# Optimization experiments

Hardware: AMD Instinct MI355X
Metric: run time of the kernel (lower is better)

Reference implementation:

```python
import jax, jax.numpy as jnp
import numpy as np

NUM_FREQS = 12  # fourfeat_config
EMB_DIM = 3 + 6 * NUM_FREQS  # identity + sin/cos per freq per dim = 75


def fourier_ipe(x, cov, decay):
    # x: [N,3], cov: [N,3,3], decay: scalar (coarse-to-fine window cutoff)
    N = x.shape[0]
    freqs = 2.0 ** jnp.arange(NUM_FREQS, dtype=jnp.float32)            # [F]
    xb = x[:, None, :] * freqs[:, None]                                # [N,F,3]
    var = jnp.diagonal(cov, axis1=-2, axis2=-1)[:, None, :] * (freqs ** 2)[:, None]  # [N,F,3]
    # nerfies-style cosine easing window per frequency band
    window = 0.5 * (1.0 - jnp.cos(jnp.pi * jnp.clip(decay - jnp.arange(NUM_FREQS, dtype=jnp.float32), 0.0, 1.0)))  # [F]
    atten = jnp.exp(-0.5 * var) * window[:, None]                      # [N,F,3]
    four = jnp.concatenate([jnp.sin(xb), jnp.cos(xb)], axis=-1) * jnp.concatenate([atten, atten], axis=-1)  # [N,F,6]
    return jnp.concatenate([x, four.reshape(N, 6 * NUM_FREQS)], axis=-1)  # [N,75]


def mlp(h, W_in, b_in, W_hid, b_hid, W_out, b_out):
    h = jax.nn.relu(h @ W_in + b_in)
    for i in range(W_hid.shape[0]):  # fixed small layer count
        h = jax.nn.relu(h @ W_hid[i] + b_hid[i])
    return h @ W_out + b_out  # output_activation = None


def setup_inputs() -> dict:
    key = jax.random.key(0)
    ks = jax.random.split(key, 16)
    bshape = (2, 16384, 8)
    mean = jax.random.normal(ks[0], (*bshape, 3), jnp.float32)
    cov = jax.random.uniform(ks[1], (*bshape, 3, 3), jnp.float32) * 1e-4  # small positive diag

    def w(k, shp):
        return jax.random.normal(k, shp, jnp.float32) / np.sqrt(shp[-2]).astype(np.float32)

    FD, FC = 256, 128  # features_density, features_color
    HD, HC = 8 - 2, 4 - 2  # n_hidden_layers = layers - 2
    return {
        'mean': mean, 'cov': cov,
        'Wd_in': w(ks[2], (EMB_DIM, FD)), 'bd_in': jnp.zeros((FD,), jnp.float32),
        'Wd_hid': w(ks[3], (HD, FD, FD)), 'bd_hid': jnp.zeros((HD, FD), jnp.float32),
        'Wd_out': w(ks[4], (FD, FD + 1)), 'bd_out': jnp.zeros((FD + 1,), jnp.float32),
        'Wc_in': w(ks[5], (FD, FC)), 'bc_in': jnp.zeros((FC,), jnp.float32),
        'Wc_hid': w(ks[6], (HC, FC, FC)), 'bc_hid': jnp.zeros((HC, FC), jnp.float32),
        'Wc_out': w(ks[7], (FC, 3)), 'bc_out': jnp.zeros((3,), jnp.float32),
        'decayscale': 12,
    }


def reference(mean, cov, Wd_in, bd_in, Wd_hid, bd_hid, Wd_out, bd_out,
              Wc_in, bc_in, Wc_hid, bc_hid, Wc_out, bc_out, decayscale):
    batch_shape = mean.shape[:-1]
    N = int(np.prod(batch_shape))
    x = mean.reshape(N, 3)
    c = cov.reshape(N, 3, 3)
    emb = fourier_ipe(x, c, jnp.float32(decayscale))                    # [N,75]
    feat = mlp(emb, Wd_in, bd_in, Wd_hid, bd_hid, Wd_out, bd_out)       # [N,257]
    d, features = feat[:, :1], feat[:, 1:]
    # parameterization == 'VolSDF' (capitalized) -> no SDF radius offset branch
    raw_rgb = mlp(features, Wc_in, bc_in, Wc_hid, bc_hid, Wc_out, bc_out)  # [N,3]
    raw = jnp.concatenate([raw_rgb, d], axis=-1)                        # [N,4]
    return raw.reshape(*batch_shape, 4)
```

## Files before the change

kernel.cpp:

```cpp
#include <hip/hip_runtime.h>
#include <hip/hip_bf16.h>

#define PI_F 3.14159265358979323846f
#define KPAD 260

typedef _Float16 h8 __attribute__((ext_vector_type(8)));
typedef _Float16 h4 __attribute__((ext_vector_type(4)));
typedef _Float16 h2 __attribute__((ext_vector_type(2)));
typedef __fp16 fp16x2 __attribute__((ext_vector_type(2)));
typedef float f32x16 __attribute__((ext_vector_type(16)));

__device__ __forceinline__ h2 cvt_pk_h2(float a, float b)
{
    fp16x2 r = __builtin_amdgcn_cvt_pkrtz(a, b);
    return __builtin_bit_cast(h2, r);
}

#define OFF_DIN   0
#define OFF_DHID  24576
#define OFF_FEAT  417792
#define OFF_CIN   483328
#define OFF_CHID  516096
#define OFF_COUT  548864
#define W_TOTAL   552960
#define FB_DIN  0
#define FB_DHID 256
#define FB_FEAT 1792
#define FB_CIN  2048
#define FB_CHID 2176
#define FB_WD0  2432
#define FB_BD0  2688
#define B_TOTAL 2689
#define PREP_TOTAL (W_TOTAL + B_TOTAL)

__global__ void prep_kernel(const float* __restrict__ Wd_in,  const float* __restrict__ Wd_hid,
                            const float* __restrict__ Wd_out, const float* __restrict__ Wc_in,
                            const float* __restrict__ Wc_hid, const float* __restrict__ Wc_out,
                            const float* __restrict__ bd_in,  const float* __restrict__ bd_hid,
                            const float* __restrict__ bd_out, const float* __restrict__ bc_in,
                            const float* __restrict__ bc_hid,
                            _Float16* __restrict__ wdst, float* __restrict__ bdst)
{
    int i = blockIdx.x * 256 + threadIdx.x;
    if (i >= PREP_TOTAL) return;
    if (i < W_TOTAL) {
        float v = 0.f;
        int j, n, k;
        #define DECODE(jj, KTv)  do { int frag = (jj) >> 3; int e = (jj) & 7;          \
                                      int lane = frag & 63; int tk = frag >> 6;         \
                                      int ntl = tk / (KTv); int kt = tk % (KTv);        \
                                      n = ntl * 32 + (lane & 31);                       \
                                      k = kt * 16 + (lane >> 5) * 8 + e; } while (0)
        if (i < OFF_DHID) {
            j = i; DECODE(j, 6);
            if (k < 75) v = Wd_in[k * 256 + n];
        } else if (i < OFF_FEAT) {
            j = i - OFF_DHID; int l = j >> 16; j &= 65535; DECODE(j, 16);
            v = Wd_hid[(l * 256 + k) * 256 + n];
        } else if (i < OFF_CIN) {
            j = i - OFF_FEAT; DECODE(j, 16);
            v = Wd_out[k * 257 + n + 1];
        } else if (i < OFF_CHID) {
            j = i - OFF_CIN; DECODE(j, 16);
            v = Wc_in[k * 128 + n];
        } else if (i < OFF_COUT) {
            j = i - OFF_CHID; int l = j >> 14; j &= 16383; DECODE(j, 8);
            v = Wc_hid[(l * 128 + k) * 128 + n];
        } else {
            j = i - OFF_COUT; DECODE(j, 8);
            if (n < 3) v = Wc_out[k * 3 + n];
        }
        #undef DECODE
        wdst[i] = (_Float16)v;
    } else {
        int b = i - W_TOTAL;
        float v = 0.f;
        #define BDECODE(bb) int ntl = (bb) >> 5; int r5 = (bb) & 31;                   \
                            int lq = r5 >> 4, jj = r5 & 15;                            \
                            int n = ntl * 32 + (jj & 3) + 8 * (jj >> 2) + 4 * lq
        if (b < FB_DHID)      { BDECODE(b); v = bd_in[n]; }
        else if (b < FB_FEAT) { int b2 = b - FB_DHID; int l = b2 >> 8; int bb = b2 & 255;
                                BDECODE(bb); v = bd_hid[l * 256 + n]; }
        else if (b < FB_CIN)  { int bb = b - FB_FEAT; BDECODE(bb); v = bd_out[n + 1]; }
        else if (b < FB_CHID) { int bb = b - FB_CIN; BDECODE(bb); v = bc_in[n]; }
        else if (b < FB_WD0)  { int b2 = b - FB_CHID; int l = b2 >> 7; int bb = b2 & 127;
                                BDECODE(bb); v = bc_hid[l * 128 + n]; }
        else if (b < FB_BD0)  { int k = b - FB_WD0; v = Wd_out[k * 257]; }
        else                  { v = bd_out[0]; }
        #undef BDECODE
        bdst[b] = v;
    }
}

__device__ __forceinline__ h8 lds_read_h8(const _Float16* p)
{
    h4 lo = *(const h4*)(p);
    h4 hi = *(const h4*)(p + 4);
    return __builtin_shufflevector(lo, hi, 0, 1, 2, 3, 4, 5, 6, 7);
}

template<int KT, int NT, bool RELU, bool DDOT>
__device__ __forceinline__ void dense(_Float16 (*At)[KPAD],
                                      const _Float16* __restrict__ WP,
                                      const float* __restrict__ bfrag,
                                      const float* __restrict__ wd0,
                                      float (*dpart)[64],
                                      int c, int lrow, int lq, int lane)
{
    const int ntile0 = c * NT;
    f32x16 acc[2][NT];
#pragma unroll
    for (int nt = 0; nt < NT; ++nt) {
        f32x16 b = *(const f32x16*)(bfrag + (ntile0 + nt) * 32 + lq * 16);
        acc[0][nt] = b;
        acc[1][nt] = b;
    }

    const _Float16* wbase = WP + ((size_t)ntile0 * KT) * 512 + (size_t)lane * 8;

#pragma unroll 2
    for (int kt = 0; kt < KT; ++kt) {
        const int koff = kt * 16 + lq * 8;
        h8 wf[NT];
#pragma unroll
        for (int nt = 0; nt < NT; ++nt)
            wf[nt] = *(const h8*)(wbase + (size_t)(nt * KT + kt) * 512);
        h8 af[2];
#pragma unroll
        for (int mt = 0; mt < 2; ++mt)
            af[mt] = lds_read_h8(&At[mt * 32 + lrow][koff]);
        __builtin_amdgcn_s_setprio(1);
#pragma unroll
        for (int mt = 0; mt < 2; ++mt)
#pragma unroll
            for (int nt = 0; nt < NT; ++nt)
                acc[mt][nt] = __builtin_amdgcn_mfma_f32_32x32x16_f16(wf[nt], af[mt], acc[mt][nt], 0, 0, 0);
        __builtin_amdgcn_s_setprio(0);
    }

    if (DDOT) {
        float s = 0.f;
        const float* w0 = wd0 + c * 64;
#pragma unroll
        for (int kk = 0; kk < 64; kk += 8) {
            h8 hv = lds_read_h8(&At[lane][c * 64 + kk]);
#pragma unroll
            for (int e = 0; e < 8; ++e)
                s = fmaf((float)hv[e], w0[kk + e], s);
        }
        dpart[c][lane] = s;
    }

    __syncthreads();

#pragma unroll
    for (int mt = 0; mt < 2; ++mt) {
        const int m = mt * 32 + lrow;
#pragma unroll
        for (int nt = 0; nt < NT; ++nt) {
#pragma unroll
            for (int p = 0; p < 4; ++p) {
                const int n0 = (ntile0 + nt) * 32 + p * 8 + lq * 4;
                h2 lo = cvt_pk_h2(acc[mt][nt][4 * p + 0], acc[mt][nt][4 * p + 1]);
                h2 hi = cvt_pk_h2(acc[mt][nt][4 * p + 2], acc[mt][nt][4 * p + 3]);
                h4 hv = __builtin_shufflevector(lo, hi, 0, 1, 2, 3);
                if (RELU) {
                    const h4 zero = {(_Float16)0, (_Float16)0, (_Float16)0, (_Float16)0};
                    hv = __builtin_elementwise_max(hv, zero);
                }
                *(h4*)(&At[m][n0]) = hv;
            }
        }
    }
    __syncthreads();
}

__global__ __launch_bounds__(256, 4)
void ffmlp_kernel(const float* __restrict__ mean, const float* __restrict__ cov,
                  const int* __restrict__ decayscale,
                  const _Float16* __restrict__ wws, const float* __restrict__ bws,
                  const float* __restrict__ bc_out,
                  float* __restrict__ out, int N)
{
    __shared__ __align__(16) _Float16 At[64][KPAD];
    __shared__ float dpart[4][64];

    const int t = threadIdx.x;
    const int c = t >> 6, lane = t & 63;
    const int lrow = lane & 31, lq = lane >> 5;
    const int p0 = blockIdx.x * 64;

    {
        const int m = t >> 2, q = t & 3;
        const long pt = (long)p0 + m;
        float x0 = 0.f, x1 = 0.f, x2 = 0.f, v0 = 0.f, v1 = 0.f, v2 = 0.f;
        if (pt < N) {
            x0 = mean[pt * 3 + 0]; x1 = mean[pt * 3 + 1]; x2 = mean[pt * 3 + 2];
            v0 = cov[pt * 9 + 0];  v1 = cov[pt * 9 + 4];  v2 = cov[pt * 9 + 8];
        }
        const float dec = (float)(*decayscale);
        if (q == 0) {
            At[m][0] = (_Float16)x0; At[m][1] = (_Float16)x1; At[m][2] = (_Float16)x2;
            for (int k = 75; k < 80; ++k) At[m][k] = (_Float16)0.f;
        } else {
            for (int k = 75 + 5 * q; k < (q == 3 ? 96 : 80 + 5 * q); ++k) At[m][k] = (_Float16)0.f;
        }
        const float xs[3] = {x0, x1, x2}, vs[3] = {v0, v1, v2};
#pragma unroll
        for (int fi = 0; fi < 3; ++fi) {
            const int f = q * 3 + fi;
            const float fs = (float)(1 << f);
            const float wcl = fminf(fmaxf(dec - (float)f, 0.f), 1.f);
            const float win = 0.5f * (1.f - cosf(wcl * PI_F));
#pragma unroll
            for (int d = 0; d < 3; ++d) {
                const float xb = xs[d] * fs;
                const float att = expf(-0.5f * vs[d] * fs * fs) * win;
                float s, co;
                sincosf(xb, &s, &co);
                At[m][3 + 6 * f + d] = (_Float16)(s * att);
                At[m][6 + 6 * f + d] = (_Float16)(co * att);
            }
        }
    }
    __syncthreads();

    dense<6, 2, true, false>(At, wws + OFF_DIN, bws + FB_DIN, bws, dpart, c, lrow, lq, lane);
#pragma unroll 1
    for (int i = 0; i < 6; ++i)
        dense<16, 2, true, false>(At, wws + OFF_DHID + i * 65536, bws + FB_DHID + i * 256,
                                  bws, dpart, c, lrow, lq, lane);
    dense<16, 2, false, true>(At, wws + OFF_FEAT, bws + FB_FEAT, bws + FB_WD0, dpart, c, lrow, lq, lane);

    dense<16, 1, true, false>(At, wws + OFF_CIN, bws + FB_CIN, bws, dpart, c, lrow, lq, lane);
#pragma unroll 1
    for (int i = 0; i < 2; ++i)
        dense<8, 1, true, false>(At, wws + OFF_CHID + i * 16384, bws + FB_CHID + i * 128,
                                 bws, dpart, c, lrow, lq, lane);

    if (c == 0) {
        f32x16 acc[2];
#pragma unroll
        for (int mt = 0; mt < 2; ++mt)
#pragma unroll
            for (int j = 0; j < 16; ++j) acc[mt][j] = 0.f;
        const _Float16* wco = wws + OFF_COUT + (size_t)lane * 8;
#pragma unroll
        for (int kt = 0; kt < 8; ++kt) {
            const int koff = kt * 16 + lq * 8;
            h8 wf = *(const h8*)(wco + (size_t)kt * 512);
#pragma unroll
            for (int mt = 0; mt < 2; ++mt) {
                h8 af = lds_read_h8(&At[mt * 32 + lrow][koff]);
                acc[mt] = __builtin_amdgcn_mfma_f32_32x32x16_f16(wf, af, acc[mt], 0, 0, 0);
            }
        }
        const float bc0 = bc_out[0], bc1 = bc_out[1], bc2 = bc_out[2];
        const float bd0 = bws[FB_BD0];
        if (lq == 0) {
#pragma unroll
            for (int mt = 0; mt < 2; ++mt) {
                const int m = mt * 32 + lrow;
                const long pt = (long)p0 + m;
                if (pt < N) {
                    float4 o;
                    o.x = acc[mt][0] + bc0;
                    o.y = acc[mt][1] + bc1;
                    o.z = acc[mt][2] + bc2;
                    o.w = dpart[0][m] + dpart[1][m] + dpart[2][m] + dpart[3][m] + bd0;
                    *(float4*)(out + pt * 4) = o;
                }
            }
        }
    }
}

extern "C" void kernel_launch(void* const* d_in, const int* in_sizes, int n_in,
                              void* d_out, int out_size, void* d_ws, size_t ws_size,
                              hipStream_t stream)
{
    const float* mean   = (const float*)d_in[0];
    const float* cov    = (const float*)d_in[1];
    const float* Wd_in  = (const float*)d_in[2];
    const float* bd_in  = (const float*)d_in[3];
    const float* Wd_hid = (const float*)d_in[4];
    const float* bd_hid = (const float*)d_in[5];
    const float* Wd_out = (const float*)d_in[6];
    const float* bd_out = (const float*)d_in[7];
    const float* Wc_in  = (const float*)d_in[8];
    const float* bc_in  = (const float*)d_in[9];
    const float* Wc_hid = (const float*)d_in[10];
    const float* bc_hid = (const float*)d_in[11];
    const float* Wc_out = (const float*)d_in[12];
    const float* bc_out = (const float*)d_in[13];
    const int*   decay  = (const int*)d_in[14];

    _Float16* wws = (_Float16*)d_ws;
    float*    bws = (float*)((char*)d_ws + (size_t)W_TOTAL * 2);

    const int N = in_sizes[0] / 3;

    const int prep_blocks = (PREP_TOTAL + 255) / 256;
    prep_kernel<<<prep_blocks, 256, 0, stream>>>(Wd_in, Wd_hid, Wd_out, Wc_in, Wc_hid, Wc_out,
                                                 bd_in, bd_hid, bd_out, bc_in, bc_hid, wws, bws);

    const int blocks = (N + 63) / 64;
    ffmlp_kernel<<<blocks, 256, 0, stream>>>(mean, cov, decay, wws, bws, bc_out, (float*)d_out, N);
}
```

Measured before the change: 315.1 us.

## Enlarge block tile to 128 rows with 2x2 wave grid for weight reuse

Each block now processes 128 points instead of 64. The four waves are arranged as two row groups by two column groups, so each wave computes 64 rows by a wider N slice (NT doubled). This halves the global weight fetches per point and increases MFMA work per weight load. In exchange it doubles LDS and accumulator registers, lowers the occupancy hint from 4 to 2 blocks per CU, and halves the block count. The DDOT and final-layer paths are reindexed to match.

```diff
diff --git a/kernel.cpp b/kernel.cpp
--- a/kernel.cpp
+++ b/kernel.cpp
@@ -104,10 +104,10 @@
                                       const _Float16* __restrict__ WP,
                                       const float* __restrict__ bfrag,
                                       const float* __restrict__ wd0,
-                                      float (*dpart)[64],
-                                      int c, int lrow, int lq, int lane)
-{
-    const int ntile0 = c * NT;
+                                      float (*dpart)[128],
+                                      int rbase, int ntile0, int wid,
+                                      int lrow, int lq, int lane)
+{
     f32x16 acc[2][NT];
 #pragma unroll
     for (int nt = 0; nt < NT; ++nt) {
@@ -128,7 +128,7 @@
         h8 af[2];
 #pragma unroll
         for (int mt = 0; mt < 2; ++mt)
-            af[mt] = lds_read_h8(&At[mt * 32 + lrow][koff]);
+            af[mt] = lds_read_h8(&At[rbase + mt * 32 + lrow][koff]);
         __builtin_amdgcn_s_setprio(1);
 #pragma unroll
         for (int mt = 0; mt < 2; ++mt)
@@ -139,23 +139,27 @@
     }
 
     if (DDOT) {
-        float s = 0.f;
-        const float* w0 = wd0 + c * 64;
-#pragma unroll
-        for (int kk = 0; kk < 64; kk += 8) {
-            h8 hv = lds_read_h8(&At[lane][c * 64 + kk]);
-#pragma unroll
-            for (int e = 0; e < 8; ++e)
-                s = fmaf((float)hv[e], w0[kk + e], s);
-        }
-        dpart[c][lane] = s;
+        const float* w0 = wd0 + wid * 64;
+#pragma unroll
+        for (int m2 = 0; m2 < 2; ++m2) {
+            const int m = lane + m2 * 64;
+            float s = 0.f;
+#pragma unroll
+            for (int kk = 0; kk < 64; kk += 8) {
+                h8 hv = lds_read_h8(&At[m][wid * 64 + kk]);
+#pragma unroll
+                for (int e = 0; e < 8; ++e)
+                    s = fmaf((float)hv[e], w0[kk + e], s);
+            }
+            dpart[wid][m] = s;
+        }
     }
 
     __syncthreads();
 
 #pragma unroll
     for (int mt = 0; mt < 2; ++mt) {
-        const int m = mt * 32 + lrow;
+        const int m = rbase + mt * 32 + lrow;
 #pragma unroll
         for (int nt = 0; nt < NT; ++nt) {
 #pragma unroll
@@ -175,23 +179,25 @@
     __syncthreads();
 }
 
-__global__ __launch_bounds__(256, 4)
+__global__ __launch_bounds__(256, 2)
 void ffmlp_kernel(const float* __restrict__ mean, const float* __restrict__ cov,
                   const int* __restrict__ decayscale,
                   const _Float16* __restrict__ wws, const float* __restrict__ bws,
                   const float* __restrict__ bc_out,
                   float* __restrict__ out, int N)
 {
-    __shared__ __align__(16) _Float16 At[64][KPAD];
-    __shared__ float dpart[4][64];
+    __shared__ __align__(16) _Float16 At[128][KPAD];
+    __shared__ float dpart[4][128];
 
     const int t = threadIdx.x;
-    const int c = t >> 6, lane = t & 63;
+    const int wid = t >> 6, lane = t & 63;
+    const int r = wid >> 1, c = wid & 1;
     const int lrow = lane & 31, lq = lane >> 5;
-    const int p0 = blockIdx.x * 64;
+    const int rbase = r * 64;
+    const int p0 = blockIdx.x * 128;
 
     {
-        const int m = t >> 2, q = t & 3;
+        const int m = t >> 1, hf = t & 1;
         const long pt = (long)p0 + m;
         float x0 = 0.f, x1 = 0.f, x2 = 0.f, v0 = 0.f, v1 = 0.f, v2 = 0.f;
         if (pt < N) {
@@ -199,16 +205,16 @@
             v0 = cov[pt * 9 + 0];  v1 = cov[pt * 9 + 4];  v2 = cov[pt * 9 + 8];
         }
         const float dec = (float)(*decayscale);
-        if (q == 0) {
+        if (hf == 0) {
             At[m][0] = (_Float16)x0; At[m][1] = (_Float16)x1; At[m][2] = (_Float16)x2;
-            for (int k = 75; k < 80; ++k) At[m][k] = (_Float16)0.f;
+            for (int k = 75; k < 86; ++k) At[m][k] = (_Float16)0.f;
         } else {
-            for (int k = 75 + 5 * q; k < (q == 3 ? 96 : 80 + 5 * q); ++k) At[m][k] = (_Float16)0.f;
+            for (int k = 86; k < 96; ++k) At[m][k] = (_Float16)0.f;
         }
         const float xs[3] = {x0, x1, x2}, vs[3] = {v0, v1, v2};
 #pragma unroll
-        for (int fi = 0; fi < 3; ++fi) {
-            const int f = q * 3 + fi;
+        for (int fi = 0; fi < 6; ++fi) {
+            const int f = hf * 6 + fi;
             const float fs = (float)(1 << f);
             const float wcl = fminf(fmaxf(dec - (float)f, 0.f), 1.f);
             const float win = 0.5f * (1.f - cosf(wcl * PI_F));
@@ -225,18 +231,21 @@
     }
     __syncthreads();
 
-    dense<6, 2, true, false>(At, wws + OFF_DIN, bws + FB_DIN, bws, dpart, c, lrow, lq, lane);
+    dense<6, 4, true, false>(At, wws + OFF_DIN, bws + FB_DIN, bws, dpart,
+                             rbase, c * 4, wid, lrow, lq, lane);
 #pragma unroll 1
     for (int i = 0; i < 6; ++i)
-        dense<16, 2, true, false>(At, wws + OFF_DHID + i * 65536, bws + FB_DHID + i * 256,
-                                  bws, dpart, c, lrow, lq, lane);
-    dense<16, 2, false, true>(At, wws + OFF_FEAT, bws + FB_FEAT, bws + FB_WD0, dpart, c, lrow, lq, lane);
-
-    dense<16, 1, true, false>(At, wws + OFF_CIN, bws + FB_CIN, bws, dpart, c, lrow, lq, lane);
+        dense<16, 4, true, false>(At, wws + OFF_DHID + i * 65536, bws + FB_DHID + i * 256,
+                                  bws, dpart, rbase, c * 4, wid, lrow, lq, lane);
+    dense<16, 4, false, true>(At, wws + OFF_FEAT, bws + FB_FEAT, bws + FB_WD0, dpart,
+                              rbase, c * 4, wid, lrow, lq, lane);
+
+    dense<16, 2, true, false>(At, wws + OFF_CIN, bws + FB_CIN, bws, dpart,
+                              rbase, c * 2, wid, lrow, lq, lane);
 #pragma unroll 1
     for (int i = 0; i < 2; ++i)
-        dense<8, 1, true, false>(At, wws + OFF_CHID + i * 16384, bws + FB_CHID + i * 128,
-                                 bws, dpart, c, lrow, lq, lane);
+        dense<8, 2, true, false>(At, wws + OFF_CHID + i * 16384, bws + FB_CHID + i * 128,
+                                 bws, dpart, rbase, c * 2, wid, lrow, lq, lane);
 
     if (c == 0) {
         f32x16 acc[2];
@@ -251,7 +260,7 @@
             h8 wf = *(const h8*)(wco + (size_t)kt * 512);
 #pragma unroll
             for (int mt = 0; mt < 2; ++mt) {
-                h8 af = lds_read_h8(&At[mt * 32 + lrow][koff]);
+                h8 af = lds_read_h8(&At[rbase + mt * 32 + lrow][koff]);
                 acc[mt] = __builtin_amdgcn_mfma_f32_32x32x16_f16(wf, af, acc[mt], 0, 0, 0);
             }
         }
@@ -260,7 +269,7 @@
         if (lq == 0) {
 #pragma unroll
             for (int mt = 0; mt < 2; ++mt) {
-                const int m = mt * 32 + lrow;
+                const int m = rbase + mt * 32 + lrow;
                 const long pt = (long)p0 + m;
                 if (pt < N) {
                     float4 o;
@@ -304,6 +313,6 @@
     prep_kernel<<<prep_blocks, 256, 0, stream>>>(Wd_in, Wd_hid, Wd_out, Wc_in, Wc_hid, Wc_out,
                                                  bd_in, bd_hid, bd_out, bc_in, bc_hid, wws, bws);
 
-    const int blocks = (N + 63) / 64;
+    const int blocks = (N + 127) / 128;
     ffmlp_kernel<<<blocks, 256, 0, stream>>>(mean, cov, decay, wws, bws, bc_out, (float*)d_out, N);
 }
```

Result: faster. 307.1 us (-2.6%).

## Double-buffer weight fragments into LDS via async global_load_lds prefetch

Applied to the files above, without the earlier changes.

Weight fragments are no longer loaded straight from global memory into registers. Each wave now uses asynchronous global-to-LDS loads into a private double buffer, prefetching the next k-tile while MFMAs run on the current one, with explicit vmcnt waits. The intent is to hide global or L2 weight-load latency behind the MFMA work. It costs 16 KB of extra LDS per block and lowers the launch-bounds occupancy hint from 4 to 3. It also depends on correct LDS ordering without a barrier, which holds only because each wave has its own buffer.

```diff
diff --git a/kernel.cpp b/kernel.cpp
--- a/kernel.cpp
+++ b/kernel.cpp
@@ -14,6 +14,13 @@
 {
     fp16x2 r = __builtin_amdgcn_cvt_pkrtz(a, b);
     return __builtin_bit_cast(h2, r);
+}
+
+__device__ __forceinline__ void stage16(const _Float16* g, _Float16* l)
+{
+    __builtin_amdgcn_global_load_lds(
+        (const __attribute__((address_space(1))) unsigned int*)g,
+        (__attribute__((address_space(3))) unsigned int*)l, 16, 0, 0);
 }
 
 #define OFF_DIN   0
@@ -101,6 +108,7 @@
 
 template<int KT, int NT, bool RELU, bool DDOT>
 __device__ __forceinline__ void dense(_Float16 (*At)[KPAD],
+                                      _Float16* __restrict__ wb,
                                       const _Float16* __restrict__ WP,
                                       const float* __restrict__ bfrag,
                                       const float* __restrict__ wd0,
@@ -116,15 +124,28 @@
         acc[1][nt] = b;
     }
 
-    const _Float16* wbase = WP + ((size_t)ntile0 * KT) * 512 + (size_t)lane * 8;
+#pragma unroll
+    for (int nt = 0; nt < NT; ++nt)
+        stage16(WP + ((size_t)((ntile0 + nt) * KT)) * 512 + lane * 8, wb + nt * 512);
 
 #pragma unroll 2
     for (int kt = 0; kt < KT; ++kt) {
+        if (kt + 1 < KT) {
+#pragma unroll
+            for (int nt = 0; nt < NT; ++nt)
+                stage16(WP + ((size_t)((ntile0 + nt) * KT + kt + 1)) * 512 + lane * 8,
+                        wb + ((kt + 1) & 1) * 1024 + nt * 512);
+            if constexpr (NT == 2) asm volatile("s_waitcnt vmcnt(2)" ::: "memory");
+            else                   asm volatile("s_waitcnt vmcnt(1)" ::: "memory");
+        } else {
+            asm volatile("s_waitcnt vmcnt(0)" ::: "memory");
+        }
+
         const int koff = kt * 16 + lq * 8;
         h8 wf[NT];
 #pragma unroll
         for (int nt = 0; nt < NT; ++nt)
-            wf[nt] = *(const h8*)(wbase + (size_t)(nt * KT + kt) * 512);
+            wf[nt] = *(const h8*)(wb + (kt & 1) * 1024 + nt * 512 + lane * 8);
         h8 af[2];
 #pragma unroll
         for (int mt = 0; mt < 2; ++mt)
@@ -175,7 +196,7 @@
     __syncthreads();
 }
 
-__global__ __launch_bounds__(256, 4)
+__global__ __launch_bounds__(256, 3)
 void ffmlp_kernel(const float* __restrict__ mean, const float* __restrict__ cov,
                   const int* __restrict__ decayscale,
                   const _Float16* __restrict__ wws, const float* __restrict__ bws,
@@ -183,12 +204,14 @@
                   float* __restrict__ out, int N)
 {
     __shared__ __align__(16) _Float16 At[64][KPAD];
+    __shared__ __align__(16) _Float16 wbuf[4][2][1024];
     __shared__ float dpart[4][64];
 
     const int t = threadIdx.x;
     const int c = t >> 6, lane = t & 63;
     const int lrow = lane & 31, lq = lane >> 5;
     const int p0 = blockIdx.x * 64;
+    _Float16* wb = &wbuf[c][0][0];
 
     {
         const int m = t >> 2, q = t & 3;
@@ -225,17 +248,18 @@
     }
     __syncthreads();
 
-    dense<6, 2, true, false>(At, wws + OFF_DIN, bws + FB_DIN, bws, dpart, c, lrow, lq, lane);
+    dense<6, 2, true, false>(At, wb, wws + OFF_DIN, bws + FB_DIN, bws, dpart, c, lrow, lq, lane);
 #pragma unroll 1
     for (int i = 0; i < 6; ++i)
-        dense<16, 2, true, false>(At, wws + OFF_DHID + i * 65536, bws + FB_DHID + i * 256,
+        dense<16, 2, true, false>(At, wb, wws + OFF_DHID + i * 65536, bws + FB_DHID + i * 256,
                                   bws, dpart, c, lrow, lq, lane);
-    dense<16, 2, false, true>(At, wws + OFF_FEAT, bws + FB_FEAT, bws + FB_WD0, dpart, c, lrow, lq, lane);
-
-    dense<16, 1, true, false>(At, wws + OFF_CIN, bws + FB_CIN, bws, dpart, c, lrow, lq, lane);
+    dense<16, 2, false, true>(At, wb, wws + OFF_FEAT, bws + FB_FEAT, bws + FB_WD0, dpart,
+                              c, lrow, lq, lane);
+
+    dense<16, 1, true, false>(At, wb, wws + OFF_CIN, bws + FB_CIN, bws, dpart, c, lrow, lq, lane);
 #pragma unroll 1
     for (int i = 0; i < 2; ++i)
-        dense<8, 1, true, false>(At, wws + OFF_CHID + i * 16384, bws + FB_CHID + i * 128,
+        dense<8, 1, true, false>(At, wb, wws + OFF_CHID + i * 16384, bws + FB_CHID + i * 128,
                                  bws, dpart, c, lrow, lq, lane);
 
     if (c == 0) {
```

New measurement: 355.7 us. 12.9% more time.

## Double-buffer weight and activation fragments across k-phases in dense layers

Applied to the files above, without the earlier changes.

Restructures the dense-layer k-loop into phases of several k-tiles with a two-slot register buffer. The global weight loads and LDS activation reads for the next phase are issued before the MFMAs of the current phase, so memory latency can overlap with matrix math. Launch bounds are relaxed from 4 to 2 blocks per SM to leave room for the larger register footprint. This trades occupancy for per-wave latency hiding.

```diff
diff --git a/kernel.cpp b/kernel.cpp
--- a/kernel.cpp
+++ b/kernel.cpp
@@ -99,7 +99,7 @@
     return __builtin_shufflevector(lo, hi, 0, 1, 2, 3, 4, 5, 6, 7);
 }
 
-template<int KT, int NT, bool RELU, bool DDOT>
+template<int KT, int PH, int NT, bool RELU, bool DDOT>
 __device__ __forceinline__ void dense(_Float16 (*At)[KPAD],
                                       const _Float16* __restrict__ WP,
                                       const float* __restrict__ bfrag,
@@ -107,7 +107,10 @@
                                       float (*dpart)[64],
                                       int c, int lrow, int lq, int lane)
 {
+    constexpr int NPH = KT / PH;
+    static_assert(NPH * PH == KT, "PH must divide KT");
     const int ntile0 = c * NT;
+
     f32x16 acc[2][NT];
 #pragma unroll
     for (int nt = 0; nt < NT; ++nt) {
@@ -116,25 +119,45 @@
         acc[1][nt] = b;
     }
 
-    const _Float16* wbase = WP + ((size_t)ntile0 * KT) * 512 + (size_t)lane * 8;
-
-#pragma unroll 2
-    for (int kt = 0; kt < KT; ++kt) {
-        const int koff = kt * 16 + lq * 8;
-        h8 wf[NT];
+    const _Float16* wbase  = WP + ((size_t)ntile0 * KT) * 512 + (size_t)lane * 8;
+    const _Float16* abase0 = &At[lrow][lq * 8];
+    const _Float16* abase1 = &At[32 + lrow][lq * 8];
+
+    h8 wfb[2][NT * PH];
+    h8 afb[2][2 * PH];
+
+#pragma unroll
+    for (int kk = 0; kk < PH; ++kk) {
 #pragma unroll
         for (int nt = 0; nt < NT; ++nt)
-            wf[nt] = *(const h8*)(wbase + (size_t)(nt * KT + kt) * 512);
-        h8 af[2];
-#pragma unroll
-        for (int mt = 0; mt < 2; ++mt)
-            af[mt] = lds_read_h8(&At[mt * 32 + lrow][koff]);
+            wfb[0][nt * PH + kk] = *(const h8*)(wbase + (size_t)(nt * KT + kk) * 512);
+        afb[0][kk]      = lds_read_h8(abase0 + kk * 16);
+        afb[0][PH + kk] = lds_read_h8(abase1 + kk * 16);
+    }
+
+#pragma unroll
+    for (int ph = 0; ph < NPH; ++ph) {
+        const int cur = ph & 1, nxt = cur ^ 1;
+        if (ph + 1 < NPH) {
+#pragma unroll
+            for (int kk = 0; kk < PH; ++kk) {
+                const int kt = (ph + 1) * PH + kk;
+#pragma unroll
+                for (int nt = 0; nt < NT; ++nt)
+                    wfb[nxt][nt * PH + kk] = *(const h8*)(wbase + (size_t)(nt * KT + kt) * 512);
+                afb[nxt][kk]      = lds_read_h8(abase0 + kt * 16);
+                afb[nxt][PH + kk] = lds_read_h8(abase1 + kt * 16);
+            }
+        }
         __builtin_amdgcn_s_setprio(1);
 #pragma unroll
-        for (int mt = 0; mt < 2; ++mt)
-#pragma unroll
-            for (int nt = 0; nt < NT; ++nt)
-                acc[mt][nt] = __builtin_amdgcn_mfma_f32_32x32x16_f16(wf[nt], af[mt], acc[mt][nt], 0, 0, 0);
+        for (int kk = 0; kk < PH; ++kk)
+#pragma unroll
+            for (int mt = 0; mt < 2; ++mt)
+#pragma unroll
+                for (int nt = 0; nt < NT; ++nt)
+                    acc[mt][nt] = __builtin_amdgcn_mfma_f32_32x32x16_f16(
+                        wfb[cur][nt * PH + kk], afb[cur][mt * PH + kk], acc[mt][nt], 0, 0, 0);
         __builtin_amdgcn_s_setprio(0);
     }
 
@@ -175,7 +198,7 @@
     __syncthreads();
 }
 
-__global__ __launch_bounds__(256, 4)
+__global__ __launch_bounds__(256, 2)
 void ffmlp_kernel(const float* __restrict__ mean, const float* __restrict__ cov,
                   const int* __restrict__ decayscale,
                   const _Float16* __restrict__ wws, const float* __restrict__ bws,
@@ -225,18 +248,19 @@
     }
     __syncthreads();
 
-    dense<6, 2, true, false>(At, wws + OFF_DIN, bws + FB_DIN, bws, dpart, c, lrow, lq, lane);
+    dense<6, 3, 2, true, false>(At, wws + OFF_DIN, bws + FB_DIN, bws, dpart, c, lrow, lq, lane);
 #pragma unroll 1
     for (int i = 0; i < 6; ++i)
-        dense<16, 2, true, false>(At, wws + OFF_DHID + i * 65536, bws + FB_DHID + i * 256,
-                                  bws, dpart, c, lrow, lq, lane);
-    dense<16, 2, false, true>(At, wws + OFF_FEAT, bws + FB_FEAT, bws + FB_WD0, dpart, c, lrow, lq, lane);
-
-    dense<16, 1, true, false>(At, wws + OFF_CIN, bws + FB_CIN, bws, dpart, c, lrow, lq, lane);
+        dense<16, 4, 2, true, false>(At, wws + OFF_DHID + i * 65536, bws + FB_DHID + i * 256,
+                                     bws, dpart, c, lrow, lq, lane);
+    dense<16, 4, 2, false, true>(At, wws + OFF_FEAT, bws + FB_FEAT, bws + FB_WD0, dpart,
+                                 c, lrow, lq, lane);
+
+    dense<16, 4, 1, true, false>(At, wws + OFF_CIN, bws + FB_CIN, bws, dpart, c, lrow, lq, lane);
 #pragma unroll 1
     for (int i = 0; i < 2; ++i)
-        dense<8, 1, true, false>(At, wws + OFF_CHID + i * 16384, bws + FB_CHID + i * 128,
-                                 bws, dpart, c, lrow, lq, lane);
+        dense<8, 4, 1, true, false>(At, wws + OFF_CHID + i * 16384, bws + FB_CHID + i * 128,
+                                    bws, dpart, c, lrow, lq, lane);
 
     if (c == 0) {
         f32x16 acc[2];
```

New measurement: 319.4 us. No clear change (+1.4%).
